# Performance work log

Hardware: AMD Instinct MI355X
Metric: run time of the kernel (lower is better)

The kernel has to match this reference:

```python
import jax, jax.numpy as jnp
import numpy as np

N = 100000   # nodes
E = 800000   # edges (avg degree 8)
IN_DIM = 384
HID = 256
BN_EPS = 1e-5


def setup_inputs() -> dict:
    key = jax.random.key(0)
    ks = jax.random.split(key, 12)
    x = jax.random.normal(ks[0], (N, IN_DIM), dtype=jnp.float32)
    edge_index = jax.random.randint(ks[1], (2, E), 0, N, dtype=jnp.int32)
    # GCNConv params (glorot-ish scaling)
    W1 = jax.random.normal(ks[2], (IN_DIM, HID), dtype=jnp.float32) * (1.0 / np.sqrt(IN_DIM))
    b1 = jnp.zeros((HID,), jnp.float32)
    W2 = jax.random.normal(ks[3], (HID, HID), dtype=jnp.float32) * (1.0 / np.sqrt(HID))
    b2 = jnp.zeros((HID,), jnp.float32)
    # BatchNorm affine params
    g1 = jnp.ones((HID,), jnp.float32)
    be1 = jnp.zeros((HID,), jnp.float32)
    g2 = jnp.ones((HID,), jnp.float32)
    be2 = jnp.zeros((HID,), jnp.float32)
    return {"x": x, "edge_index": edge_index, "W1": W1, "b1": b1, "g1": g1,
            "be1": be1, "W2": W2, "b2": b2, "g2": g2, "be2": be2}


def _gcn_conv(x, W, b, src, dst):
    """PyG GCNConv: self-loops + symmetric normalization D^-1/2 A D^-1/2."""
    h = x @ W                                             # [N, H]
    deg = jnp.zeros((x.shape[0],), h.dtype).at[dst].add(1.0) + 1.0  # in-deg + self loop
    dinv = jax.lax.rsqrt(deg)                             # [N]
    coef = dinv[src] * dinv[dst]                          # [E]
    agg = jnp.zeros_like(h).at[dst].add(h[src] * coef[:, None])     # scatter-add messages
    agg = agg + h * (1.0 / deg)[:, None]                  # self-loop term (norm = 1/deg)
    return agg + b


def _batchnorm(h, gamma, beta):
    # training-mode BN over node dim, biased variance (matches torch normalization)
    mu = jnp.mean(h, axis=0)
    var = jnp.mean(jnp.square(h - mu), axis=0)
    return gamma * (h - mu) * jax.lax.rsqrt(var + BN_EPS) + beta


def reference(x, edge_index, W1, b1, g1, be1, W2, b2, g2, be2):
    src, dst = edge_index[0], edge_index[1]
    h = _gcn_conv(x, W1, b1, src, dst)
    h = jax.nn.relu(_batchnorm(h, g1, be1))
    # dropout: eval mode -> identity
    h = _gcn_conv(h, W2, b2, src, dst)
    h = jax.nn.relu(_batchnorm(h, g2, be2))
    return h
```

## Files before the change

### kernel.cpp

```cpp
#include <hip/hip_runtime.h>
#include <hip/hip_bf16.h>

#define NN  100000
#define NE  800000
#define KIN 384
#define HID 256
#define BN_EPS 1e-5f

typedef __attribute__((ext_vector_type(4))) float floatx4;
typedef __attribute__((ext_vector_type(8))) short short8;

__device__ __forceinline__ unsigned short f2b(float f) {
    union { float f; unsigned int u; } v; v.f = f;
    unsigned int r = v.u + 0x7fffu + ((v.u >> 16) & 1u);
    return (unsigned short)(r >> 16);
}
__device__ __forceinline__ float b2f(unsigned short h) {
    union { unsigned int u; float f; } v; v.u = ((unsigned int)h) << 16;
    return v.f;
}

__global__ void k_wt2(const float* __restrict__ W1, unsigned short* __restrict__ W1t,
                      const float* __restrict__ W2, unsigned short* __restrict__ W2t) {
    const int n = threadIdx.x;
    const int k = blockIdx.x;
    if (k < KIN) W1t[(size_t)n * KIN + k] = f2b(W1[(size_t)k * HID + n]);
    else {
        const int k2 = k - KIN;
        W2t[(size_t)n * HID + k2] = f2b(W2[(size_t)k2 * HID + n]);
    }
}

__global__ void k_count(const int* __restrict__ dst, int* __restrict__ deg) {
    int i = blockIdx.x * 256 + threadIdx.x;
    if (i < NE) atomicAdd(deg + dst[i], 1);
}

__device__ __forceinline__ int block_incl_scan(int v, int* lds) {
    lds[threadIdx.x] = v; __syncthreads();
    #pragma unroll
    for (int off = 1; off < 256; off <<= 1) {
        int t = lds[threadIdx.x];
        int a = (threadIdx.x >= off) ? lds[threadIdx.x - off] : 0;
        __syncthreads();
        lds[threadIdx.x] = t + a;
        __syncthreads();
    }
    return lds[threadIdx.x];
}

__global__ __launch_bounds__(256) void k_scan1(const int* __restrict__ deg,
                                               int* __restrict__ bsum,
                                               float* __restrict__ dinv) {
    __shared__ int lds[256];
    int i = blockIdx.x * 256 + threadIdx.x;
    int v = (i < NN) ? deg[i] : 0;
    if (i < NN) dinv[i] = rsqrtf((float)(v + 1));
    int incl = block_incl_scan(v, lds);
    if (threadIdx.x == 255) bsum[blockIdx.x] = incl;
}

__global__ __launch_bounds__(512) void k_scan2(const int* __restrict__ bsum,
                                               int* __restrict__ boff, int nb,
                                               int* __restrict__ rowptr) {
    __shared__ int lds[512];
    int v = (threadIdx.x < nb) ? bsum[threadIdx.x] : 0;
    lds[threadIdx.x] = v; __syncthreads();
    #pragma unroll
    for (int off = 1; off < 512; off <<= 1) {
        int t = lds[threadIdx.x];
        int a = (threadIdx.x >= off) ? lds[threadIdx.x - off] : 0;
        __syncthreads();
        lds[threadIdx.x] = t + a;
        __syncthreads();
    }
    if (threadIdx.x < nb) boff[threadIdx.x] = lds[threadIdx.x] - v;
    if (threadIdx.x == 0) rowptr[NN] = NE;
}

__global__ __launch_bounds__(256) void k_scan3(const int* __restrict__ deg,
                                               const int* __restrict__ boff,
                                               int* __restrict__ rowptr) {
    __shared__ int lds[256];
    int i = blockIdx.x * 256 + threadIdx.x;
    int v = (i < NN) ? deg[i] : 0;
    int incl = block_incl_scan(v, lds);
    if (i < NN) rowptr[i] = incl - v + boff[blockIdx.x];
}

__global__ __launch_bounds__(256) void k_fill(
    const int* __restrict__ src, const int* __restrict__ dst,
    const float* __restrict__ dinv, const int* __restrict__ rowptr,
    int* __restrict__ cursor, int2* __restrict__ epk)
{
    int e = blockIdx.x * 256 + threadIdx.x;
    if (e < NE) {
        const int d = dst[e], s = src[e];
        const int pos = rowptr[d] + atomicAdd(cursor + d, 1);
        int2 rec; rec.x = s; rec.y = __float_as_int(dinv[s]);
        epk[pos] = rec;
    }
}

template<int K, int MODE, int ABF16>
__global__ __launch_bounds__(512) void k_gemm(
    const void* __restrict__ Av, const unsigned short* __restrict__ Bt,
    unsigned short* __restrict__ C,
    const float* __restrict__ bnacc, const float* __restrict__ g,
    const float* __restrict__ be, int M)
{
    constexpr int BM = 128, BK = 32, LD = 40;
    __shared__ __align__(16) unsigned short As[BM * LD];
    __shared__ __align__(16) unsigned short Bs[HID * LD];
    __shared__ float s_sc[HID], s_bi[HID];
    const int tid = threadIdx.x;
    const int lane = tid & 63;
    const int wid  = tid >> 6;
    const int wm = wid & 1, wn = wid >> 1;
    const int l15 = lane & 15, lq = lane >> 4;
    const int row0 = blockIdx.x * BM;

    if (MODE) {
        if (tid < HID) {
            const float inv_n = 1.f / (float)NN;
            const float mu  = bnacc[tid] * inv_n;
            const float var = bnacc[HID + tid] * inv_n - mu * mu;
            const float s   = g[tid] * rsqrtf(var + BN_EPS);
            s_sc[tid] = s;
            s_bi[tid] = be[tid] - s * mu;
        }
        __syncthreads();
    }

    floatx4 acc[4][4] = {};

    const int ar  = tid >> 3;
    const int ak  = (tid & 7) * 4;
    const int ar2 = tid >> 2;
    const int ak2 = (tid & 3) * 8;
    const int bn_ = tid >> 2;
    const int bk  = (tid & 3) * 8;

    for (int k0 = 0; k0 < K; k0 += BK) {
        if (ABF16) {
            const unsigned short* A = (const unsigned short*)Av;
            const int grow = row0 + ar2;
            float x[8];
            if (grow < M) {
                short8 v = *(const short8*)(A + (size_t)grow * K + k0 + ak2);
                #pragma unroll
                for (int t = 0; t < 8; ++t) x[t] = b2f((unsigned short)v[t]);
                if (MODE) {
                    float4 s0 = *(const float4*)(s_sc + k0 + ak2);
                    float4 s1 = *(const float4*)(s_sc + k0 + ak2 + 4);
                    float4 b0 = *(const float4*)(s_bi + k0 + ak2);
                    float4 b1 = *(const float4*)(s_bi + k0 + ak2 + 4);
                    x[0] = fmaxf(x[0] * s0.x + b0.x, 0.f);
                    x[1] = fmaxf(x[1] * s0.y + b0.y, 0.f);
                    x[2] = fmaxf(x[2] * s0.z + b0.z, 0.f);
                    x[3] = fmaxf(x[3] * s0.w + b0.w, 0.f);
                    x[4] = fmaxf(x[4] * s1.x + b1.x, 0.f);
                    x[5] = fmaxf(x[5] * s1.y + b1.y, 0.f);
                    x[6] = fmaxf(x[6] * s1.z + b1.z, 0.f);
                    x[7] = fmaxf(x[7] * s1.w + b1.w, 0.f);
                }
            } else {
                #pragma unroll
                for (int t = 0; t < 8; ++t) x[t] = 0.f;
            }
            short8 o;
            #pragma unroll
            for (int t = 0; t < 8; ++t) o[t] = (short)f2b(x[t]);
            *(short8*)(As + ar2 * LD + ak2) = o;
        } else {
            const float* A = (const float*)Av;
            #pragma unroll
            for (int p = 0; p < 2; ++p) {
                const int row  = p * 64 + ar;
                const int grow = row0 + row;
                float x0 = 0.f, x1 = 0.f, x2 = 0.f, x3 = 0.f;
                if (grow < M) {
                    float4 v = *(const float4*)(A + (size_t)grow * K + k0 + ak);
                    x0 = v.x; x1 = v.y; x2 = v.z; x3 = v.w;
                }
                ushort4 o;
                o.x = f2b(x0); o.y = f2b(x1); o.z = f2b(x2); o.w = f2b(x3);
                *(ushort4*)(As + row * LD + ak) = o;
            }
        }
        #pragma unroll
        for (int p = 0; p < 2; ++p) {
            const int n = p * 128 + bn_;
            *(float4*)(Bs + n * LD + bk) =
                *(const float4*)(Bt + (size_t)n * K + k0 + bk);
        }
        __syncthreads();

        short8 af[4], bf[4];
        #pragma unroll
        for (int i = 0; i < 4; ++i)
            af[i] = *(const short8*)(As + (wm * 64 + i * 16 + l15) * LD + lq * 8);
        #pragma unroll
        for (int j = 0; j < 4; ++j)
            bf[j] = *(const short8*)(Bs + (wn * 64 + j * 16 + l15) * LD + lq * 8);
        #pragma unroll
        for (int i = 0; i < 4; ++i)
            #pragma unroll
            for (int j = 0; j < 4; ++j)
                acc[i][j] = __builtin_amdgcn_mfma_f32_16x16x32_bf16(af[i], bf[j], acc[i][j], 0, 0, 0);
        __syncthreads();
    }

    #pragma unroll
    for (int i = 0; i < 4; ++i) {
        #pragma unroll
        for (int r = 0; r < 4; ++r) {
            const int m = row0 + wm * 64 + i * 16 + lq * 4 + r;
            if (m < M) {
                #pragma unroll
                for (int j = 0; j < 4; ++j) {
                    const int c = wn * 64 + j * 16 + l15;
                    C[(size_t)m * HID + c] = f2b(acc[i][j][r]);
                }
            }
        }
    }
}

__global__ __launch_bounds__(256, 6) void k_gather(
    const unsigned short* __restrict__ H, const int2* __restrict__ epk,
    const int* __restrict__ rowptr, const float* __restrict__ dinv,
    unsigned short* __restrict__ AGGb, float* __restrict__ bn_acc)
{
    __shared__ float ls[512];
    const int tid = threadIdx.x, lane = tid & 63, w = tid >> 6;
    const int half = lane >> 5;
    const int l32  = lane & 31;
    const int c0   = l32 * 8;
    float s[8] = {}, q[8] = {};

    for (int n = blockIdx.x * 4 + w; n < NN; n += gridDim.x * 4) {
        const int beg = rowptr[n], end = rowptr[n + 1];
        const float di = dinv[n];
        float a[8] = {};
        int j = beg;
        for (; j + 8 <= end; j += 8) {
            #pragma unroll
            for (int t = 0; t < 4; ++t) {
                const int2 e = epk[j + half + 2 * t];
                const float cf = __int_as_float(e.y) * di;
                const short8 h = *(const short8*)(H + (size_t)e.x * HID + c0);
                #pragma unroll
                for (int u = 0; u < 8; ++u)
                    a[u] += b2f((unsigned short)h[u]) * cf;
            }
        }
        for (; j + 2 <= end; j += 2) {
            const int2 e = epk[j + half];
            const float cf = __int_as_float(e.y) * di;
            const short8 h = *(const short8*)(H + (size_t)e.x * HID + c0);
            #pragma unroll
            for (int u = 0; u < 8; ++u)
                a[u] += b2f((unsigned short)h[u]) * cf;
        }
        if (j < end && half == 0) {
            const int2 e = epk[j];
            const float cf = __int_as_float(e.y) * di;
            const short8 h = *(const short8*)(H + (size_t)e.x * HID + c0);
            #pragma unroll
            for (int u = 0; u < 8; ++u)
                a[u] += b2f((unsigned short)h[u]) * cf;
        }
        if (half == 1) {
            const float cs = di * di;
            const short8 h = *(const short8*)(H + (size_t)n * HID + c0);
            #pragma unroll
            for (int u = 0; u < 8; ++u)
                a[u] += b2f((unsigned short)h[u]) * cs;
        }
        #pragma unroll
        for (int u = 0; u < 8; ++u)
            a[u] += __shfl_xor(a[u], 32);
        if (half == 0) {
            short8 o;
            #pragma unroll
            for (int u = 0; u < 8; ++u) o[u] = (short)f2b(a[u]);
            *(short8*)(AGGb + (size_t)n * HID + c0) = o;
            #pragma unroll
            for (int u = 0; u < 8; ++u) { s[u] += a[u]; q[u] += a[u] * a[u]; }
        }
    }

    ls[tid] = 0.f; ls[tid + 256] = 0.f;
    __syncthreads();
    if (half == 0) {
        #pragma unroll
        for (int u = 0; u < 8; ++u) {
            atomicAdd(&ls[c0 + u], s[u]);
            atomicAdd(&ls[256 + c0 + u], q[u]);
        }
    }
    __syncthreads();
    atomicAdd(bn_acc + tid, ls[tid]);
    atomicAdd(bn_acc + 256 + tid, ls[tid + 256]);
}

__global__ __launch_bounds__(256) void k_apply(
    const unsigned short* __restrict__ AGGb, const float* __restrict__ bnacc,
    const float* __restrict__ g, const float* __restrict__ be,
    float* __restrict__ out)
{
    const int gid = blockIdx.x * 256 + threadIdx.x;
    if (gid < NN * (HID / 4)) {
        const int c4 = (gid & 63) * 4;
        float sc[4], bi[4];
        const float inv_n = 1.f / (float)NN;
        #pragma unroll
        for (int u = 0; u < 4; ++u) {
            const int c = c4 + u;
            const float mu  = bnacc[c] * inv_n;
            const float var = bnacc[HID + c] * inv_n - mu * mu;
            const float sv  = g[c] * rsqrtf(var + BN_EPS);
            sc[u] = sv; bi[u] = be[c] - sv * mu;
        }
        ushort4 v = *(const ushort4*)(AGGb + (size_t)gid * 4);
        float4 o;
        o.x = fmaxf(b2f(v.x) * sc[0] + bi[0], 0.f);
        o.y = fmaxf(b2f(v.y) * sc[1] + bi[1], 0.f);
        o.z = fmaxf(b2f(v.z) * sc[2] + bi[2], 0.f);
        o.w = fmaxf(b2f(v.w) * sc[3] + bi[3], 0.f);
        *(float4*)(out + (size_t)gid * 4) = o;
    }
}

extern "C" void kernel_launch(void* const* d_in, const int* in_sizes, int n_in,
                              void* d_out, int out_size, void* d_ws, size_t ws_size,
                              hipStream_t stream)
{
    const float* x   = (const float*)d_in[0];
    const int*   ei  = (const int*)d_in[1];
    const float* W1  = (const float*)d_in[2];
    const float* g1  = (const float*)d_in[4];
    const float* be1 = (const float*)d_in[5];
    const float* W2  = (const float*)d_in[6];
    const float* g2  = (const float*)d_in[8];
    const float* be2 = (const float*)d_in[9];
    float* out = (float*)d_out;
    const int* srcp = ei;
    const int* dstp = ei + NE;

    constexpr int NB = (NN + 255) / 256;

    char* p = (char*)d_ws;
    int*            deg    = (int*)p;             p += (size_t)NN * 4;
    int*            cursor = (int*)p;             p += (size_t)NN * 4;
    float*          bn1    = (float*)p;           p += 512 * 4;
    float*          bn2    = (float*)p;           p += 512 * 4;
    const size_t zbytes = (size_t)NN * 8 + 4096;
    unsigned short* AGGb   = (unsigned short*)p;  p += (size_t)NN * HID * 2;
    unsigned short* H      = (unsigned short*)p;  p += (size_t)NN * HID * 2;
    float*          dinv   = (float*)p;           p += (size_t)NN * 4;
    int*            rowptr = (int*)p;             p += (size_t)(NN + 1) * 4;
    int2*           epk    = (int2*)p;            p += (size_t)NE * 8;
    int*            bsum   = (int*)p;             p += 512 * 4;
    int*            boff   = (int*)p;             p += 512 * 4;
    unsigned short* W1t    = (unsigned short*)p;  p += (size_t)KIN * HID * 2;
    unsigned short* W2t    = (unsigned short*)p;  p += (size_t)HID * HID * 2;

    hipMemsetAsync(deg, 0, zbytes, stream);

    k_wt2<<<KIN + HID, HID, 0, stream>>>(W1, W1t, W2, W2t);

    k_count<<<(NE + 255) / 256, 256, 0, stream>>>(dstp, deg);
    k_scan1<<<NB, 256, 0, stream>>>(deg, bsum, dinv);
    k_scan2<<<1, 512, 0, stream>>>(bsum, boff, NB, rowptr);
    k_scan3<<<NB, 256, 0, stream>>>(deg, boff, rowptr);
    k_fill<<<(NE + 255) / 256, 256, 0, stream>>>(srcp, dstp, dinv, rowptr, cursor, epk);

    const int ggrid = (NN + 127) / 128;

    k_gemm<KIN, 0, 0><<<ggrid, 512, 0, stream>>>(x, W1t, H, nullptr, nullptr, nullptr, NN);
    k_gather<<<1536, 256, 0, stream>>>(H, epk, rowptr, dinv, AGGb, bn1);

    k_gemm<HID, 1, 1><<<ggrid, 512, 0, stream>>>(AGGb, W2t, H, bn1, g1, be1, NN);
    k_gather<<<1536, 256, 0, stream>>>(H, epk, rowptr, dinv, AGGb, bn2);
    k_apply<<<(NN * (HID / 4) + 255) / 256, 256, 0, stream>>>(AGGb, bn2, g2, be2, out);
}
```

Measured before the change: 661.1 us.

## Prefetch GEMM tiles, load B via global_load_lds, batch gather loads, merge prep kernels

```diff
diff --git a/kernel.cpp b/kernel.cpp
--- a/kernel.cpp
+++ b/kernel.cpp
@@ -20,20 +20,27 @@
     return v.f;
 }
 
-__global__ void k_wt2(const float* __restrict__ W1, unsigned short* __restrict__ W1t,
-                      const float* __restrict__ W2, unsigned short* __restrict__ W2t) {
-    const int n = threadIdx.x;
-    const int k = blockIdx.x;
-    if (k < KIN) W1t[(size_t)n * KIN + k] = f2b(W1[(size_t)k * HID + n]);
-    else {
-        const int k2 = k - KIN;
-        W2t[(size_t)n * HID + k2] = f2b(W2[(size_t)k2 * HID + n]);
-    }
-}
-
-__global__ void k_count(const int* __restrict__ dst, int* __restrict__ deg) {
-    int i = blockIdx.x * 256 + threadIdx.x;
-    if (i < NE) atomicAdd(deg + dst[i], 1);
+__device__ __forceinline__ void gload_lds16(const void* g, void* l) {
+    __builtin_amdgcn_global_load_lds(
+        (const __attribute__((address_space(1))) void*)g,
+        (__attribute__((address_space(3))) void*)l, 16, 0, 0);
+}
+
+__global__ __launch_bounds__(256) void k_prep0(
+    const float* __restrict__ W1, unsigned short* __restrict__ W1t,
+    const float* __restrict__ W2, unsigned short* __restrict__ W2t,
+    const int* __restrict__ dst, int* __restrict__ deg)
+{
+    const int b = blockIdx.x;
+    if (b < KIN) {
+        W1t[(size_t)threadIdx.x * KIN + b] = f2b(W1[(size_t)b * HID + threadIdx.x]);
+    } else if (b < KIN + HID) {
+        const int k2 = b - KIN;
+        W2t[(size_t)threadIdx.x * HID + k2] = f2b(W2[(size_t)k2 * HID + threadIdx.x]);
+    } else {
+        const int i = (b - KIN - HID) * 256 + threadIdx.x;
+        if (i < NE) atomicAdd(deg + dst[i], 1);
+    }
 }
 
 __device__ __forceinline__ int block_incl_scan(int v, int* lds) {
@@ -109,9 +116,9 @@
     const float* __restrict__ bnacc, const float* __restrict__ g,
     const float* __restrict__ be, int M)
 {
-    constexpr int BM = 128, BK = 32, LD = 40;
-    __shared__ __align__(16) unsigned short As[BM * LD];
-    __shared__ __align__(16) unsigned short Bs[HID * LD];
+    constexpr int BM = 128, BK = 32, LDA = 40, LDB = 32;
+    __shared__ __align__(16) unsigned short As[BM * LDA];
+    __shared__ __align__(16) unsigned short Bs[HID * LDB];
     __shared__ float s_sc[HID], s_bi[HID];
     const int tid = threadIdx.x;
     const int lane = tid & 63;
@@ -138,71 +145,88 @@
     const int ak  = (tid & 7) * 4;
     const int ar2 = tid >> 2;
     const int ak2 = (tid & 3) * 8;
-    const int bn_ = tid >> 2;
-    const int bk  = (tid & 3) * 8;
+    const int lofs = (wid << 11) + lane * 16;
+    int brow[2], bcol[2];
+    #pragma unroll
+    for (int r = 0; r < 2; ++r) {
+        const int la = lofs + (r << 10);
+        brow[r] = la >> 6;
+        bcol[r] = (la & 63) >> 1;
+    }
+
+    float4 apf0, apf1;
+    short8 apf2 = {};
+    if (ABF16) {
+        const unsigned short* A = (const unsigned short*)Av;
+        const int grow = row0 + ar2;
+        if (grow < M) apf2 = *(const short8*)(A + (size_t)grow * K + ak2);
+    } else {
+        const float* A = (const float*)Av;
+        const int g0 = row0 + ar, g1 = row0 + 64 + ar;
+        apf0 = (g0 < M) ? *(const float4*)(A + (size_t)g0 * K + ak) : make_float4(0.f,0.f,0.f,0.f);
+        apf1 = (g1 < M) ? *(const float4*)(A + (size_t)g1 * K + ak) : make_float4(0.f,0.f,0.f,0.f);
+    }
 
     for (int k0 = 0; k0 < K; k0 += BK) {
+        #pragma unroll
+        for (int r = 0; r < 2; ++r)
+            gload_lds16(Bt + (size_t)brow[r] * K + k0 + bcol[r],
+                        (char*)Bs + lofs + (r << 10));
+
         if (ABF16) {
-            const unsigned short* A = (const unsigned short*)Av;
-            const int grow = row0 + ar2;
             float x[8];
-            if (grow < M) {
-                short8 v = *(const short8*)(A + (size_t)grow * K + k0 + ak2);
-                #pragma unroll
-                for (int t = 0; t < 8; ++t) x[t] = b2f((unsigned short)v[t]);
-                if (MODE) {
-                    float4 s0 = *(const float4*)(s_sc + k0 + ak2);
-                    float4 s1 = *(const float4*)(s_sc + k0 + ak2 + 4);
-                    float4 b0 = *(const float4*)(s_bi + k0 + ak2);
-                    float4 b1 = *(const float4*)(s_bi + k0 + ak2 + 4);
-                    x[0] = fmaxf(x[0] * s0.x + b0.x, 0.f);
-                    x[1] = fmaxf(x[1] * s0.y + b0.y, 0.f);
-                    x[2] = fmaxf(x[2] * s0.z + b0.z, 0.f);
-                    x[3] = fmaxf(x[3] * s0.w + b0.w, 0.f);
-                    x[4] = fmaxf(x[4] * s1.x + b1.x, 0.f);
-                    x[5] = fmaxf(x[5] * s1.y + b1.y, 0.f);
-                    x[6] = fmaxf(x[6] * s1.z + b1.z, 0.f);
-                    x[7] = fmaxf(x[7] * s1.w + b1.w, 0.f);
-                }
-            } else {
-                #pragma unroll
-                for (int t = 0; t < 8; ++t) x[t] = 0.f;
+            #pragma unroll
+            for (int t = 0; t < 8; ++t) x[t] = b2f((unsigned short)apf2[t]);
+            if (MODE) {
+                float4 s0 = *(const float4*)(s_sc + k0 + ak2);
+                float4 s1 = *(const float4*)(s_sc + k0 + ak2 + 4);
+                float4 b0 = *(const float4*)(s_bi + k0 + ak2);
+                float4 b1 = *(const float4*)(s_bi + k0 + ak2 + 4);
+                x[0] = fmaxf(x[0] * s0.x + b0.x, 0.f);
+                x[1] = fmaxf(x[1] * s0.y + b0.y, 0.f);
+                x[2] = fmaxf(x[2] * s0.z + b0.z, 0.f);
+                x[3] = fmaxf(x[3] * s0.w + b0.w, 0.f);
+                x[4] = fmaxf(x[4] * s1.x + b1.x, 0.f);
+                x[5] = fmaxf(x[5] * s1.y + b1.y, 0.f);
+                x[6] = fmaxf(x[6] * s1.z + b1.z, 0.f);
+                x[7] = fmaxf(x[7] * s1.w + b1.w, 0.f);
             }
             short8 o;
             #pragma unroll
             for (int t = 0; t < 8; ++t) o[t] = (short)f2b(x[t]);
-            *(short8*)(As + ar2 * LD + ak2) = o;
+            *(short8*)(As + ar2 * LDA + ak2) = o;
         } else {
-            const float* A = (const float*)Av;
-            #pragma unroll
-            for (int p = 0; p < 2; ++p) {
-                const int row  = p * 64 + ar;
-                const int grow = row0 + row;
-                float x0 = 0.f, x1 = 0.f, x2 = 0.f, x3 = 0.f;
-                if (grow < M) {
-                    float4 v = *(const float4*)(A + (size_t)grow * K + k0 + ak);
-                    x0 = v.x; x1 = v.y; x2 = v.z; x3 = v.w;
-                }
-                ushort4 o;
-                o.x = f2b(x0); o.y = f2b(x1); o.z = f2b(x2); o.w = f2b(x3);
-                *(ushort4*)(As + row * LD + ak) = o;
+            ushort4 o0, o1;
+            o0.x = f2b(apf0.x); o0.y = f2b(apf0.y); o0.z = f2b(apf0.z); o0.w = f2b(apf0.w);
+            o1.x = f2b(apf1.x); o1.y = f2b(apf1.y); o1.z = f2b(apf1.z); o1.w = f2b(apf1.w);
+            *(ushort4*)(As + ar * LDA + ak) = o0;
+            *(ushort4*)(As + (64 + ar) * LDA + ak) = o1;
+        }
+
+        const int kn = k0 + BK;
+        if (kn < K) {
+            if (ABF16) {
+                const unsigned short* A = (const unsigned short*)Av;
+                const int grow = row0 + ar2;
+                apf2 = {};
+                if (grow < M) apf2 = *(const short8*)(A + (size_t)grow * K + kn + ak2);
+            } else {
+                const float* A = (const float*)Av;
+                const int g0 = row0 + ar, g1 = row0 + 64 + ar;
+                apf0 = (g0 < M) ? *(const float4*)(A + (size_t)g0 * K + kn + ak) : make_float4(0.f,0.f,0.f,0.f);
+                apf1 = (g1 < M) ? *(const float4*)(A + (size_t)g1 * K + kn + ak) : make_float4(0.f,0.f,0.f,0.f);
             }
         }
-        #pragma unroll
-        for (int p = 0; p < 2; ++p) {
-            const int n = p * 128 + bn_;
-            *(float4*)(Bs + n * LD + bk) =
-                *(const float4*)(Bt + (size_t)n * K + k0 + bk);
-        }
+
         __syncthreads();
 
         short8 af[4], bf[4];
         #pragma unroll
         for (int i = 0; i < 4; ++i)
-            af[i] = *(const short8*)(As + (wm * 64 + i * 16 + l15) * LD + lq * 8);
+            af[i] = *(const short8*)(As + (wm * 64 + i * 16 + l15) * LDA + lq * 8);
         #pragma unroll
         for (int j = 0; j < 4; ++j)
-            bf[j] = *(const short8*)(Bs + (wn * 64 + j * 16 + l15) * LD + lq * 8);
+            bf[j] = *(const short8*)(Bs + (wn * 64 + j * 16 + l15) * LDB + lq * 8);
         #pragma unroll
         for (int i = 0; i < 4; ++i)
             #pragma unroll
@@ -227,7 +251,7 @@
     }
 }
 
-__global__ __launch_bounds__(256, 6) void k_gather(
+__global__ __launch_bounds__(256) void k_gather(
     const unsigned short* __restrict__ H, const int2* __restrict__ epk,
     const int* __restrict__ rowptr, const float* __restrict__ dinv,
     unsigned short* __restrict__ AGGb, float* __restrict__ bn_acc)
@@ -245,14 +269,18 @@
         float a[8] = {};
         int j = beg;
         for (; j + 8 <= end; j += 8) {
+            int2 e[4]; short8 h[4];
+            #pragma unroll
+            for (int t = 0; t < 4; ++t) e[t] = epk[j + half + 2 * t];
+            #pragma unroll
+            for (int t = 0; t < 4; ++t)
+                h[t] = *(const short8*)(H + (size_t)e[t].x * HID + c0);
             #pragma unroll
             for (int t = 0; t < 4; ++t) {
-                const int2 e = epk[j + half + 2 * t];
-                const float cf = __int_as_float(e.y) * di;
-                const short8 h = *(const short8*)(H + (size_t)e.x * HID + c0);
+                const float cf = __int_as_float(e[t].y) * di;
                 #pragma unroll
                 for (int u = 0; u < 8; ++u)
-                    a[u] += b2f((unsigned short)h[u]) * cf;
+                    a[u] += b2f((unsigned short)h[t][u]) * cf;
             }
         }
         for (; j + 2 <= end; j += 2) {
@@ -369,9 +397,8 @@
 
     hipMemsetAsync(deg, 0, zbytes, stream);
 
-    k_wt2<<<KIN + HID, HID, 0, stream>>>(W1, W1t, W2, W2t);
-
-    k_count<<<(NE + 255) / 256, 256, 0, stream>>>(dstp, deg);
+    k_prep0<<<KIN + HID + (NE + 255) / 256, 256, 0, stream>>>(W1, W1t, W2, W2t, dstp, deg);
+
     k_scan1<<<NB, 256, 0, stream>>>(deg, bsum, dinv);
     k_scan2<<<1, 512, 0, stream>>>(bsum, boff, NB, rowptr);
     k_scan3<<<NB, 256, 0, stream>>>(deg, boff, rowptr);
@@ -380,9 +407,9 @@
     const int ggrid = (NN + 127) / 128;
 
     k_gemm<KIN, 0, 0><<<ggrid, 512, 0, stream>>>(x, W1t, H, nullptr, nullptr, nullptr, NN);
-    k_gather<<<1536, 256, 0, stream>>>(H, epk, rowptr, dinv, AGGb, bn1);
+    k_gather<<<2560, 256, 0, stream>>>(H, epk, rowptr, dinv, AGGb, bn1);
 
     k_gemm<HID, 1, 1><<<ggrid, 512, 0, stream>>>(AGGb, W2t, H, bn1, g1, be1, NN);
-    k_gather<<<1536, 256, 0, stream>>>(H, epk, rowptr, dinv, AGGb, bn2);
+    k_gather<<<2560, 256, 0, stream>>>(H, epk, rowptr, dinv, AGGb, bn2);
     k_apply<<<(NN * (HID / 4) + 255) / 256, 256, 0, stream>>>(AGGb, bn2, g2, be2, out);
 }
```

New measurement: 699.4 us. +5.8%, slower.
